# Kernel optimization log

Measured on AMD Instinct MI355X. Metric: run time of the kernel, lower is better.

## Reference

```python
import jax, jax.numpy as jnp
import numpy as np

HIDDEN = 4096
N_HEADS = 32
N_KV_HEADS = 8
HEAD_DIM = HIDDEN // N_HEADS  # 128
Q_BITS = 8
ROPE_BASE = 10000.0


def setup_inputs() -> dict:
    key = jax.random.key(0)
    ks = jax.random.split(key, 6)
    b, s = 1, 2048
    hidden_states = jax.random.normal(ks[0], (b, s, HIDDEN), dtype=jnp.float32)
    position_ids = jnp.arange(s, dtype=jnp.int64 if jax.config.jax_enable_x64 else jnp.int32)[None, :]
    w_scale = 0.02
    wq = jax.random.normal(ks[1], (N_HEADS * HEAD_DIM, HIDDEN), dtype=jnp.float32) * w_scale
    wk = jax.random.normal(ks[2], (N_KV_HEADS * HEAD_DIM, HIDDEN), dtype=jnp.float32) * w_scale
    wv = jax.random.normal(ks[3], (N_KV_HEADS * HEAD_DIM, HIDDEN), dtype=jnp.float32) * w_scale
    wo = jax.random.normal(ks[4], (HIDDEN, N_HEADS * HEAD_DIM), dtype=jnp.float32) * w_scale
    return {"hidden_states": hidden_states, "wq": wq, "wk": wk, "wv": wv, "wo": wo,
            "position_ids": position_ids}


def _rope_tables(seq_len):
    inv_freq = 1.0 / (ROPE_BASE ** (jnp.arange(0, HEAD_DIM, 2, dtype=jnp.float32) / HEAD_DIM))
    t = jnp.arange(seq_len, dtype=jnp.float32)
    freqs = jnp.einsum('i,j->ij', t, inv_freq)          # [s, hd/2]
    emb = jnp.concatenate([freqs, freqs], axis=-1)      # [s, hd]
    return jnp.cos(emb), jnp.sin(emb)


def _rotate_half(x):
    x1, x2 = x[..., :HEAD_DIM // 2], x[..., HEAD_DIM // 2:]
    return jnp.concatenate([-x2, x1], axis=-1)


def _sym_quant_dequant(x):
    # per-token symmetric int8 quantization along head_dim (sym_quant + sym_dequant)
    q_max = 2 ** (Q_BITS - 1) - 1
    scale = jnp.clip(jnp.max(jnp.abs(x), axis=-1, keepdims=True) / q_max, 1e-9, None)
    q_int = jnp.clip(jnp.round(x / scale), -(q_max + 1), q_max)
    return q_int * scale


def reference(hidden_states, wq, wk, wv, wo, position_ids):
    b, s, _ = hidden_states.shape
    # projections -> [b, n_heads, s, head_dim]
    q = (hidden_states @ wq.T).reshape(b, s, N_HEADS, HEAD_DIM).transpose(0, 2, 1, 3)
    k = (hidden_states @ wk.T).reshape(b, s, N_KV_HEADS, HEAD_DIM).transpose(0, 2, 1, 3)
    v = (hidden_states @ wv.T).reshape(b, s, N_KV_HEADS, HEAD_DIM).transpose(0, 2, 1, 3)

    cos, sin = _rope_tables(s)
    cos = cos[position_ids][:, None]  # [b, 1, s, hd]
    sin = sin[position_ids][:, None]
    q = q * cos + _rotate_half(q) * sin
    k = k * cos + _rotate_half(k) * sin

    # int8 symmetric quantize/dequantize of K and V (KV-cache quantization)
    k = _sym_quant_dequant(k)
    v = _sym_quant_dequant(v)

    # GQA repeat_kv: [b, n_kv, s, hd] -> [b, n_heads, s, hd]
    n_rep = N_HEADS // N_KV_HEADS
    k = jnp.repeat(k, n_rep, axis=1)
    v = jnp.repeat(v, n_rep, axis=1)

    scores = jnp.einsum('bhqd,bhkd->bhqk', q, k) / jnp.sqrt(jnp.float32(HEAD_DIM))
    causal = jnp.tril(jnp.ones((s, s), dtype=bool))
    scores = jnp.where(causal, scores, jnp.float32(-1e9))
    attn = jax.nn.softmax(scores, axis=-1)

    out = jnp.einsum('bhqk,bhkd->bhqd', attn, v)
    out = out.transpose(0, 2, 1, 3).reshape(b, s, N_HEADS * HEAD_DIM)
    return out @ wo.T
```

## Files before the change

kernel.cpp:

```cpp
#include <hip/hip_runtime.h>


#define S_LEN 2048
#define HID 4096
#define NH 32
#define NKV 8
#define HD 128
#define QKV_N 6144

typedef __bf16 bf16x8 __attribute__((ext_vector_type(8)));
typedef float f32x4 __attribute__((ext_vector_type(4)));

__device__ __forceinline__ unsigned short f2b(float f) {
  unsigned int u = __float_as_uint(f);
  u += 0x7fffu + ((u >> 16) & 1u);
  return (unsigned short)(u >> 16);
}
__device__ __forceinline__ float b2f(unsigned short h) {
  return __uint_as_float(((unsigned int)h) << 16);
}
__device__ __forceinline__ void gl_lds16(const void* g, void* l) {
  __builtin_amdgcn_global_load_lds(
      (__attribute__((address_space(1))) void*)g,
      (__attribute__((address_space(3))) void*)l, 16, 0, 0);
}
__device__ __forceinline__ bf16x8 ds_read128(const void* p) {
  bf16x8 r;
  unsigned a = (unsigned)(unsigned long long)
      (__attribute__((address_space(3))) const void*)p;
  asm volatile("ds_read_b128 %0, %1" : "=v"(r) : "v"(a));
  return r;
}
__device__ __forceinline__ int swz(int row) {
  return ((row & 7) << 4) ^ (((row >> 3) & 1) << 5);
}
__device__ __forceinline__ void barrier_np() {
  asm volatile("" ::: "memory");
  __builtin_amdgcn_s_barrier();
  asm volatile("" ::: "memory");
}
#define WAITL0                                            \
  do {                                                    \
    asm volatile("s_waitcnt lgkmcnt(0)" ::: "memory");    \
    __builtin_amdgcn_sched_barrier(0);                    \
  } while (0)

__global__ __launch_bounds__(256) void cast_kernel(const float* __restrict__ src,
                                                   unsigned short* __restrict__ dst,
                                                   int n4) {
  int i = blockIdx.x * 256 + threadIdx.x;
  if (i >= n4) return;
  float4 v = ((const float4*)src)[i];
  ushort4 o;
  o.x = f2b(v.x); o.y = f2b(v.y); o.z = f2b(v.z); o.w = f2b(v.w);
  ((ushort4*)dst)[i] = o;
}

template <int BN, int CMODE>
__global__ __launch_bounds__(256, 2) void gemm_bt(const unsigned short* __restrict__ A,
                                                  const unsigned short* __restrict__ B,
                                                  void* __restrict__ Cout,
                                                  int M, int N, int K) {
  constexpr int NI = BN / 32;
  constexpr int BSTRIDE = 16384 + BN * 128;
  __shared__ __align__(16) char lds[2 * BSTRIDE];
  const int tid = threadIdx.x;
  const int lane = tid & 63, wave = tid >> 6;
  const int quad = lane >> 4, l16 = lane & 15;
  const int wave_m = wave >> 1, wave_n = wave & 1;
  const long row0 = (long)blockIdx.y * 128;
  const long col0 = (long)blockIdx.x * BN;
  const int NT = K >> 6;
  const long rowstride = (long)K * 2;

  f32x4 acc[4][NI] = {};

  auto stageA = [&](int T, int h, int buf) {
    if (T >= NT) return;
    char* dst = lds + buf * BSTRIDE + h * 8192 + wave * 1024;
    const char* src = (const char*)A + (row0 + h * 64) * rowstride + (long)T * 128;
#pragma unroll
    for (int c = 0; c < 2; ++c) {
      int b = c * 4096 + wave * 1024 + lane * 16;
      int r = b >> 7, cb = b & 127;
      gl_lds16(src + (long)r * rowstride + (cb ^ swz(r)), dst + c * 4096);
    }
  };
  auto stageB = [&](int T, int h, int buf) {
    if (T >= NT) return;
    char* dst = lds + buf * BSTRIDE + 16384 + h * (BN * 64) + wave * 1024;
    const char* src = (const char*)B + (col0 + h * (BN / 2)) * rowstride + (long)T * 128;
#pragma unroll
    for (int c = 0; c < BN / 64; ++c) {
      int b = c * 4096 + wave * 1024 + lane * 16;
      int r = b >> 7, cb = b & 127;
      gl_lds16(src + (long)r * rowstride + (cb ^ swz(r)), dst + c * 4096);
    }
  };
  auto fence_steady = [&]() {
    if (BN == 192) asm volatile("s_waitcnt vmcnt(5)" ::: "memory");
    else           asm volatile("s_waitcnt vmcnt(4)" ::: "memory");
  };

  stageA(0, 0, 0); stageB(0, 0, 0);
  stageA(0, 1, 0); stageB(0, 1, 0);
  stageA(1, 0, 1); stageB(1, 0, 1);
  fence_steady();

  for (int g = 0; g < NT; ++g) {
    const int buf = g & 1;
    barrier_np();
    stageA(g + 1, 1, buf ^ 1);
    stageB(g + 1, 1, buf ^ 1);

    bf16x8 a[2][4], b[2][NI];
#pragma unroll
    for (int mi = 0; mi < 4; ++mi) {
      int row = wave_m * 64 + mi * 16 + l16;
      const char* rp = lds + buf * BSTRIDE + row * 128;
      int sw = swz(row);
      a[0][mi] = ds_read128(rp + ((quad * 16) ^ sw));
      a[1][mi] = ds_read128(rp + ((64 + quad * 16) ^ sw));
    }
#pragma unroll
    for (int ni = 0; ni < NI; ++ni) {
      int row = wave_n * (BN / 2) + ni * 16 + l16;
      const char* rp = lds + buf * BSTRIDE + 16384 + row * 128;
      int sw = swz(row);
      b[0][ni] = ds_read128(rp + ((quad * 16) ^ sw));
      b[1][ni] = ds_read128(rp + ((64 + quad * 16) ^ sw));
    }
    WAITL0;
    barrier_np();
    stageA(g + 2, 0, buf);
    stageB(g + 2, 0, buf);

    __builtin_amdgcn_s_setprio(1);
#pragma unroll
    for (int ks = 0; ks < 2; ++ks)
#pragma unroll
      for (int mi = 0; mi < 4; ++mi)
#pragma unroll
        for (int ni = 0; ni < NI; ++ni)
          acc[mi][ni] = __builtin_amdgcn_mfma_f32_16x16x32_bf16(
              a[ks][mi], b[ks][ni], acc[mi][ni], 0, 0, 0);
    __builtin_amdgcn_s_setprio(0);

    if (g + 2 < NT) fence_steady();
    else            asm volatile("s_waitcnt vmcnt(0)" ::: "memory");
  }

#pragma unroll
  for (int mi = 0; mi < 4; ++mi)
#pragma unroll
    for (int ni = 0; ni < NI; ++ni)
#pragma unroll
      for (int r = 0; r < 4; ++r) {
        long row = row0 + wave_m * 64 + mi * 16 + quad * 4 + r;
        long col = col0 + wave_n * (BN / 2) + ni * 16 + l16;
        float v = acc[mi][ni][r];
        if (CMODE == 1) ((unsigned short*)Cout)[row * N + col] = f2b(v);
        else            ((float*)Cout)[row * N + col] = v;
      }
}

__global__ __launch_bounds__(256) void postproc(const unsigned short* __restrict__ qkv,
                                                const int* __restrict__ pos_ids,
                                                unsigned short* __restrict__ Qb,
                                                unsigned short* __restrict__ Kb,
                                                unsigned short* __restrict__ Vb) {
  const int s = blockIdx.x;
  const int lane = threadIdx.x & 63, wave = threadIdx.x >> 6;
  const float pos = (float)pos_ids[s];
  const float invf = expf(-(float)lane * 0.14391156831212787f);
  const float ang = pos * invf;
  const float ca = cosf(ang), sa = sinf(ang);

  for (int r = wave; r < 48; r += 4) {
    if (r < 32) {
      const unsigned short* src = qkv + (long)s * QKV_N + r * HD;
      float x0 = b2f(src[lane]), x1 = b2f(src[lane + 64]);
      unsigned short* dst = Qb + ((long)r * S_LEN + s) * HD;
      dst[lane]      = f2b(x0 * ca - x1 * sa);
      dst[lane + 64] = f2b(x1 * ca + x0 * sa);
    } else if (r < 40) {
      int h = r - 32;
      const unsigned short* src = qkv + (long)s * QKV_N + 4096 + h * HD;
      float x0 = b2f(src[lane]), x1 = b2f(src[lane + 64]);
      float y0 = x0 * ca - x1 * sa;
      float y1 = x1 * ca + x0 * sa;
      float m = fmaxf(fabsf(y0), fabsf(y1));
      for (int off = 32; off; off >>= 1) m = fmaxf(m, __shfl_xor(m, off, 64));
      float scale = fmaxf(m / 127.0f, 1e-9f);
      float q0 = fminf(fmaxf(rintf(y0 / scale), -128.f), 127.f);
      float q1 = fminf(fmaxf(rintf(y1 / scale), -128.f), 127.f);
      unsigned short* dst = Kb + ((long)h * S_LEN + s) * HD;
      dst[lane]      = f2b(q0 * scale);
      dst[lane + 64] = f2b(q1 * scale);
    } else {
      int h = r - 40;
      const unsigned short* src = qkv + (long)s * QKV_N + 5120 + h * HD;
      float x0 = b2f(src[lane]), x1 = b2f(src[lane + 64]);
      float m = fmaxf(fabsf(x0), fabsf(x1));
      for (int off = 32; off; off >>= 1) m = fmaxf(m, __shfl_xor(m, off, 64));
      float scale = fmaxf(m / 127.0f, 1e-9f);
      float q0 = fminf(fmaxf(rintf(x0 / scale), -128.f), 127.f);
      float q1 = fminf(fmaxf(rintf(x1 / scale), -128.f), 127.f);
      unsigned short* dst = Vb + ((long)h * S_LEN + s) * HD;
      dst[lane]      = f2b(q0 * scale);
      dst[lane + 64] = f2b(q1 * scale);
    }
  }
}

__global__ __launch_bounds__(256) void transpose_v(const unsigned short* __restrict__ Vb,
                                                   unsigned short* __restrict__ Vtb) {
  __shared__ unsigned short t[64][136];
  const int h = blockIdx.x >> 5, st = blockIdx.x & 31;
  const int tid = threadIdx.x;
  const long vbase = (long)h * S_LEN * HD;
#pragma unroll
  for (int p = 0; p < 8; ++p) {
    int e = p * 1024 + tid * 4;
    int sl = e >> 7, d = e & 127;
    ushort4 v = *(const ushort4*)(Vb + vbase + (long)(st * 64 + sl) * HD + d);
    t[sl][d] = v.x; t[sl][d + 1] = v.y; t[sl][d + 2] = v.z; t[sl][d + 3] = v.w;
  }
  __syncthreads();
  const long tbase = (long)h * HD * S_LEN;
#pragma unroll
  for (int p = 0; p < 8; ++p) {
    int o = p * 1024 + tid * 4;
    int d = o >> 6, sl = o & 63;
    ushort4 v;
    v.x = t[sl][d]; v.y = t[sl + 1][d]; v.z = t[sl + 2][d]; v.w = t[sl + 3][d];
    *(ushort4*)(Vtb + tbase + (long)d * S_LEN + st * 64 + sl) = v;
  }
}

__global__ __launch_bounds__(256, 2) void attn_kernel(const unsigned short* __restrict__ Qb,
                                                      const unsigned short* __restrict__ Kb,
                                                      const unsigned short* __restrict__ Vtb,
                                                      unsigned short* __restrict__ Ob) {
  __shared__ __align__(16) char lds[81920];

  const int bx = blockIdx.x;
  const int p8 = bx & 1;
  const int g = (bx >> 1) & 7;
  const int b8 = bx >> 8;
  const int qt = (p8 ^ b8) ? (15 - g) : g;
  const int h = ((bx >> 4) & 15) + 16 * b8;
  const int hk = h >> 2;
  const int tid = threadIdx.x;
  const int lane = tid & 63, wave = tid >> 6;
  const int quad = lane >> 4, l16 = lane & 15;

  bf16x8 qf[2][4];
  {
    const unsigned short* qb =
        Qb + ((long)h * S_LEN + qt * 128 + wave * 32 + l16) * HD + quad * 8;
#pragma unroll
    for (int mi = 0; mi < 2; ++mi)
#pragma unroll
      for (int ks = 0; ks < 4; ++ks)
        qf[mi][ks] = *(const bf16x8*)(qb + mi * 16 * HD + ks * 32);
  }

  f32x4 O[2][8] = {};
  float mrow[2][4], lrow[2][4];
#pragma unroll
  for (int mi = 0; mi < 2; ++mi)
#pragma unroll
    for (int r = 0; r < 4; ++r) { mrow[mi][r] = -1e30f; lrow[mi][r] = 0.f; }

  const char* Kg = (const char*)(Kb + (long)hk * S_LEN * HD);
  const char* Vg = (const char*)(Vtb + (long)hk * HD * S_LEN);
  char* PsB = lds + 65536;
  const float sscale = 0.08838834764831845f;
  const int nsteps = 2 * qt + 2;

  auto stageK = [&](int step, int buf) {
    char* dst = lds + buf * 16384 + wave * 1024;
    const char* src = Kg + (long)step * 16384;
#pragma unroll
    for (int c = 0; c < 4; ++c) {
      int f = c * 4096 + tid * 16;
      int row = f >> 8, wb = f & 255;
      gl_lds16(src + row * 256 + (wb ^ swz(row)), dst + c * 4096);
    }
  };
  auto stageV = [&](int step, int buf) {
    char* dst = lds + 32768 + buf * 16384 + wave * 1024;
    const char* src = Vg + (long)step * 128;
#pragma unroll
    for (int c = 0; c < 4; ++c) {
      int f = c * 4096 + tid * 16;
      int d = f >> 7, wb = f & 127;
      gl_lds16(src + (long)d * (S_LEN * 2) + (wb ^ swz(d)), dst + c * 4096);
    }
  };

  stageK(0, 0);
  stageV(0, 0);

  for (int t = 0; t < nsteps; ++t) {
    __syncthreads();
    if (t + 1 < nsteps) {
      stageK(t + 1, (t + 1) & 1);
      stageV(t + 1, (t + 1) & 1);
    }
    const char* Ks = lds + (t & 1) * 16384;
    const char* Vs = lds + 32768 + (t & 1) * 16384;

    f32x4 S[2][4] = {};
    __builtin_amdgcn_s_setprio(1);
#pragma unroll
    for (int ni = 0; ni < 4; ++ni) {
      const int row = ni * 16 + l16;
      const char* kr = Ks + row * 256;
      const int sw = swz(row);
      const int q16 = quad * 16;
      bf16x8 kf0 = *(const bf16x8*)(kr + ((q16 + 0)   ^ sw));
      bf16x8 kf1 = *(const bf16x8*)(kr + ((q16 + 64)  ^ sw));
      bf16x8 kf2 = *(const bf16x8*)(kr + ((q16 + 128) ^ sw));
      bf16x8 kf3 = *(const bf16x8*)(kr + ((q16 + 192) ^ sw));
      S[0][ni] = __builtin_amdgcn_mfma_f32_16x16x32_bf16(qf[0][0], kf0, S[0][ni], 0, 0, 0);
      S[1][ni] = __builtin_amdgcn_mfma_f32_16x16x32_bf16(qf[1][0], kf0, S[1][ni], 0, 0, 0);
      S[0][ni] = __builtin_amdgcn_mfma_f32_16x16x32_bf16(qf[0][1], kf1, S[0][ni], 0, 0, 0);
      S[1][ni] = __builtin_amdgcn_mfma_f32_16x16x32_bf16(qf[1][1], kf1, S[1][ni], 0, 0, 0);
      S[0][ni] = __builtin_amdgcn_mfma_f32_16x16x32_bf16(qf[0][2], kf2, S[0][ni], 0, 0, 0);
      S[1][ni] = __builtin_amdgcn_mfma_f32_16x16x32_bf16(qf[1][2], kf2, S[1][ni], 0, 0, 0);
      S[0][ni] = __builtin_amdgcn_mfma_f32_16x16x32_bf16(qf[0][3], kf3, S[0][ni], 0, 0, 0);
      S[1][ni] = __builtin_amdgcn_mfma_f32_16x16x32_bf16(qf[1][3], kf3, S[1][ni], 0, 0, 0);
    }
    __builtin_amdgcn_s_setprio(0);

    const bool diag = (t >= 2 * qt);
    const int qrow_base = qt * 128 + wave * 32;
    float rmax[2][4];
#pragma unroll
    for (int mi = 0; mi < 2; ++mi)
#pragma unroll
      for (int r = 0; r < 4; ++r) rmax[mi][r] = -1e30f;
#pragma unroll
    for (int mi = 0; mi < 2; ++mi)
#pragma unroll
      for (int ni = 0; ni < 4; ++ni) {
        int col = t * 64 + ni * 16 + l16;
#pragma unroll
        for (int r = 0; r < 4; ++r) {
          int row = qrow_base + mi * 16 + quad * 4 + r;
          float v = S[mi][ni][r] * sscale;
          if (diag && col > row) v = -1e9f;
          S[mi][ni][r] = v;
          rmax[mi][r] = fmaxf(rmax[mi][r], v);
        }
      }
    float alpha[2][4], rsum[2][4];
#pragma unroll
    for (int mi = 0; mi < 2; ++mi)
#pragma unroll
      for (int r = 0; r < 4; ++r) {
        float v = rmax[mi][r];
        v = fmaxf(v, __shfl_xor(v, 1, 64));
        v = fmaxf(v, __shfl_xor(v, 2, 64));
        v = fmaxf(v, __shfl_xor(v, 4, 64));
        v = fmaxf(v, __shfl_xor(v, 8, 64));
        float mnew = fmaxf(mrow[mi][r], v);
        alpha[mi][r] = __expf(mrow[mi][r] - mnew);
        mrow[mi][r] = mnew;
        rsum[mi][r] = 0.f;
      }

#pragma unroll
    for (int mi = 0; mi < 2; ++mi)
#pragma unroll
      for (int ni = 0; ni < 4; ++ni)
#pragma unroll
        for (int r = 0; r < 4; ++r) {
          float p = __expf(S[mi][ni][r] - mrow[mi][r]);
          rsum[mi][r] += p;
          int prow = wave * 32 + mi * 16 + quad * 4 + r;
          int pcol2 = (ni * 16 + l16) * 2;
          *(unsigned short*)(PsB + prow * 128 + (pcol2 ^ swz(prow))) = f2b(p);
        }
#pragma unroll
    for (int mi = 0; mi < 2; ++mi)
#pragma unroll
      for (int r = 0; r < 4; ++r) {
        float v = rsum[mi][r];
        v += __shfl_xor(v, 1, 64);
        v += __shfl_xor(v, 2, 64);
        v += __shfl_xor(v, 4, 64);
        v += __shfl_xor(v, 8, 64);
        lrow[mi][r] = lrow[mi][r] * alpha[mi][r] + v;
      }
#pragma unroll
    for (int mi = 0; mi < 2; ++mi)
#pragma unroll
      for (int ni = 0; ni < 8; ++ni)
#pragma unroll
        for (int r = 0; r < 4; ++r) O[mi][ni][r] *= alpha[mi][r];

    bf16x8 pf[2][2];
#pragma unroll
    for (int mi = 0; mi < 2; ++mi)
#pragma unroll
      for (int ks2 = 0; ks2 < 2; ++ks2) {
        int prow = wave * 32 + mi * 16 + l16;
        pf[mi][ks2] = *(const bf16x8*)(PsB + prow * 128 +
                                       ((ks2 * 64 + quad * 16) ^ swz(prow)));
      }
    __builtin_amdgcn_s_setprio(1);
#pragma unroll
    for (int ni = 0; ni < 8; ++ni) {
      const int row = ni * 16 + l16;
      const char* vr = Vs + row * 128;
      const int sw = swz(row);
      const int q16 = quad * 16;
      bf16x8 vf0 = *(const bf16x8*)(vr + ((q16 + 0)  ^ sw));
      bf16x8 vf1 = *(const bf16x8*)(vr + ((q16 + 64) ^ sw));
      O[0][ni] = __builtin_amdgcn_mfma_f32_16x16x32_bf16(pf[0][0], vf0, O[0][ni], 0, 0, 0);
      O[1][ni] = __builtin_amdgcn_mfma_f32_16x16x32_bf16(pf[1][0], vf0, O[1][ni], 0, 0, 0);
      O[0][ni] = __builtin_amdgcn_mfma_f32_16x16x32_bf16(pf[0][1], vf1, O[0][ni], 0, 0, 0);
      O[1][ni] = __builtin_amdgcn_mfma_f32_16x16x32_bf16(pf[1][1], vf1, O[1][ni], 0, 0, 0);
    }
    __builtin_amdgcn_s_setprio(0);
  }

#pragma unroll
  for (int mi = 0; mi < 2; ++mi)
#pragma unroll
    for (int r = 0; r < 4; ++r) {
      float inv = 1.0f / lrow[mi][r];
      long srow = qt * 128 + wave * 32 + mi * 16 + quad * 4 + r;
#pragma unroll
      for (int ni = 0; ni < 8; ++ni) {
        long col = (long)h * HD + ni * 16 + l16;
        Ob[srow * (long)HID + col] = f2b(O[mi][ni][r] * inv);
      }
    }
}

extern "C" void kernel_launch(void* const* d_in, const int* in_sizes, int n_in,
                              void* d_out, int out_size, void* d_ws, size_t ws_size,
                              hipStream_t stream) {
  const float* hidden = (const float*)d_in[0];
  const float* wq = (const float*)d_in[1];
  const float* wk = (const float*)d_in[2];
  const float* wv = (const float*)d_in[3];
  const float* wo = (const float*)d_in[4];
  const int* pos = (const int*)d_in[5];
  float* out = (float*)d_out;

  char* ws = (char*)d_ws;
  unsigned short* wqkv_b = (unsigned short*)(ws);
  unsigned short* wo_b   = (unsigned short*)(ws + 50331648);
  unsigned short* hid_b  = (unsigned short*)(ws + 83886080);
  unsigned short* qkv_b  = (unsigned short*)(ws + 100663296);
  unsigned short* Kb     = (unsigned short*)(ws + 125829120);
  unsigned short* Vb     = (unsigned short*)(ws + 130023424);
  unsigned short* Vtb    = (unsigned short*)(ws + 134217728);
  unsigned short* Qb     = hid_b;
  unsigned short* attn_b = qkv_b;

  cast_kernel<<<8388608 / 1024, 256, 0, stream>>>(hidden, hid_b, 8388608 / 4);
  cast_kernel<<<16777216 / 1024, 256, 0, stream>>>(wq, wqkv_b, 16777216 / 4);
  cast_kernel<<<4194304 / 1024, 256, 0, stream>>>(wk, wqkv_b + 16777216, 4194304 / 4);
  cast_kernel<<<4194304 / 1024, 256, 0, stream>>>(wv, wqkv_b + 20971520, 4194304 / 4);
  cast_kernel<<<16777216 / 1024, 256, 0, stream>>>(wo, wo_b, 16777216 / 4);

  gemm_bt<192, 1><<<dim3(QKV_N / 192, S_LEN / 128), 256, 0, stream>>>(
      hid_b, wqkv_b, (void*)qkv_b, S_LEN, QKV_N, HID);

  postproc<<<S_LEN, 256, 0, stream>>>(qkv_b, pos, Qb, Kb, Vb);
  transpose_v<<<NKV * 32, 256, 0, stream>>>(Vb, Vtb);
  attn_kernel<<<NH * 16, 256, 0, stream>>>(Qb, Kb, Vtb, attn_b);

  gemm_bt<128, 0><<<dim3(HID / 128, S_LEN / 128), 256, 0, stream>>>(
      attn_b, wo_b, (void*)out, S_LEN, HID, HID);
}
```

Measured before the change: 489.6 us.

## Single-buffer K/V via register prefetch, raise occupancy, add lazy softmax rescale

Replaces the double-buffered direct-to-LDS K/V staging with a register prefetch of the next tile that is written into a single LDS buffer after the current tile's compute. This cuts LDS use from 80KB to 48KB so launch bounds can target 3 blocks per CU. It also skips the online-softmax rescale of O and l unless some row's max grows by more than 8. The cost is an extra barrier per step, more register pressure under the tighter occupancy target, and a lazy-rescale path that lets unnormalised exponentials grow as large as e^8 before bf16 conversion.

```diff
diff --git a/kernel.cpp b/kernel.cpp
--- a/kernel.cpp
+++ b/kernel.cpp
@@ -238,11 +238,11 @@
   }
 }
 
-__global__ __launch_bounds__(256, 2) void attn_kernel(const unsigned short* __restrict__ Qb,
+__global__ __launch_bounds__(256, 3) void attn_kernel(const unsigned short* __restrict__ Qb,
                                                       const unsigned short* __restrict__ Kb,
                                                       const unsigned short* __restrict__ Vtb,
                                                       unsigned short* __restrict__ Ob) {
-  __shared__ __align__(16) char lds[81920];
+  __shared__ __align__(16) char lds[49152];
 
   const int bx = blockIdx.x;
   const int p8 = bx & 1;
@@ -275,42 +275,44 @@
 
   const char* Kg = (const char*)(Kb + (long)hk * S_LEN * HD);
   const char* Vg = (const char*)(Vtb + (long)hk * HD * S_LEN);
-  char* PsB = lds + 65536;
+  char* PsB = lds + 32768;
   const float sscale = 0.08838834764831845f;
   const int nsteps = 2 * qt + 2;
 
-  auto stageK = [&](int step, int buf) {
-    char* dst = lds + buf * 16384 + wave * 1024;
-    const char* src = Kg + (long)step * 16384;
+  int4 kpf[4], vpf[4];
+  auto loadRegs = [&](int step) {
+    const char* ks = Kg + (long)step * 16384;
+    const char* vs = Vg + (long)step * 128;
 #pragma unroll
     for (int c = 0; c < 4; ++c) {
       int f = c * 4096 + tid * 16;
-      int row = f >> 8, wb = f & 255;
-      gl_lds16(src + row * 256 + (wb ^ swz(row)), dst + c * 4096);
+      int kr = f >> 8, kb = f & 255;
+      kpf[c] = *(const int4*)(ks + kr * 256 + (kb ^ swz(kr)));
+      int d = f >> 7, vb = f & 127;
+      vpf[c] = *(const int4*)(vs + (long)d * (S_LEN * 2) + (vb ^ swz(d)));
     }
   };
-  auto stageV = [&](int step, int buf) {
-    char* dst = lds + 32768 + buf * 16384 + wave * 1024;
-    const char* src = Vg + (long)step * 128;
+  auto writeLDS = [&]() {
 #pragma unroll
     for (int c = 0; c < 4; ++c) {
-      int f = c * 4096 + tid * 16;
-      int d = f >> 7, wb = f & 127;
-      gl_lds16(src + (long)d * (S_LEN * 2) + (wb ^ swz(d)), dst + c * 4096);
+      *(int4*)(lds + c * 4096 + tid * 16) = kpf[c];
+      *(int4*)(lds + 16384 + c * 4096 + tid * 16) = vpf[c];
     }
   };
 
-  stageK(0, 0);
-  stageV(0, 0);
+  loadRegs(0);
+  asm volatile("s_waitcnt vmcnt(0)" ::: "memory");
+  writeLDS();
+  asm volatile("s_waitcnt lgkmcnt(0)" ::: "memory");
 
   for (int t = 0; t < nsteps; ++t) {
-    __syncthreads();
+    barrier_np();
     if (t + 1 < nsteps) {
-      stageK(t + 1, (t + 1) & 1);
-      stageV(t + 1, (t + 1) & 1);
-    }
-    const char* Ks = lds + (t & 1) * 16384;
-    const char* Vs = lds + 32768 + (t & 1) * 16384;
+      loadRegs(t + 1);
+      __builtin_amdgcn_sched_barrier(0);
+    }
+    const char* Ks = lds;
+    const char* Vs = lds + 16384;
 
     f32x4 S[2][4] = {};
     __builtin_amdgcn_s_setprio(1);
@@ -356,7 +358,9 @@
           rmax[mi][r] = fmaxf(rmax[mi][r], v);
         }
       }
-    float alpha[2][4], rsum[2][4];
+
+    bool need = false;
+    float pmax[2][4];
 #pragma unroll
     for (int mi = 0; mi < 2; ++mi)
 #pragma unroll
@@ -366,12 +370,29 @@
         v = fmaxf(v, __shfl_xor(v, 2, 64));
         v = fmaxf(v, __shfl_xor(v, 4, 64));
         v = fmaxf(v, __shfl_xor(v, 8, 64));
-        float mnew = fmaxf(mrow[mi][r], v);
-        alpha[mi][r] = __expf(mrow[mi][r] - mnew);
-        mrow[mi][r] = mnew;
-        rsum[mi][r] = 0.f;
+        pmax[mi][r] = v;
+        need = need || (v > mrow[mi][r] + 8.0f);
       }
-
+    if (__any(need)) {
+      float alpha[2][4];
+#pragma unroll
+      for (int mi = 0; mi < 2; ++mi)
+#pragma unroll
+        for (int r = 0; r < 4; ++r) {
+          float mnew = fmaxf(mrow[mi][r], pmax[mi][r]);
+          alpha[mi][r] = __expf(mrow[mi][r] - mnew);
+          mrow[mi][r] = mnew;
+          lrow[mi][r] *= alpha[mi][r];
+        }
+#pragma unroll
+      for (int mi = 0; mi < 2; ++mi)
+#pragma unroll
+        for (int ni = 0; ni < 8; ++ni)
+#pragma unroll
+          for (int r = 0; r < 4; ++r) O[mi][ni][r] *= alpha[mi][r];
+    }
+
+    float rsum[2][4] = {};
 #pragma unroll
     for (int mi = 0; mi < 2; ++mi)
 #pragma unroll
@@ -393,14 +414,8 @@
         v += __shfl_xor(v, 2, 64);
         v += __shfl_xor(v, 4, 64);
         v += __shfl_xor(v, 8, 64);
-        lrow[mi][r] = lrow[mi][r] * alpha[mi][r] + v;
+        lrow[mi][r] += v;
       }
-#pragma unroll
-    for (int mi = 0; mi < 2; ++mi)
-#pragma unroll
-      for (int ni = 0; ni < 8; ++ni)
-#pragma unroll
-        for (int r = 0; r < 4; ++r) O[mi][ni][r] *= alpha[mi][r];
 
     bf16x8 pf[2][2];
 #pragma unroll
@@ -426,6 +441,13 @@
       O[1][ni] = __builtin_amdgcn_mfma_f32_16x16x32_bf16(pf[1][1], vf1, O[1][ni], 0, 0, 0);
     }
     __builtin_amdgcn_s_setprio(0);
+
+    barrier_np();
+    if (t + 1 < nsteps) {
+      asm volatile("s_waitcnt vmcnt(0)" ::: "memory");
+      writeLDS();
+      asm volatile("s_waitcnt lgkmcnt(0)" ::: "memory");
+    }
   }
 
 #pragma unroll
```

Result: slower. 799.3 us (+63.3%).
